# Kernel tuning notes

Hardware: AMD Instinct MI355X
Metric: run time of the kernel (lower is better)

## Reference

```python
import jax, jax.numpy as jnp
import numpy as np

B, S, D, H, DK, DV, DFF = 2, 2048, 512, 8, 64, 64, 2048
EPS = 1e-5

def layer_norm(x, g, b):
    mu = jnp.mean(x, axis=-1, keepdims=True)
    var = jnp.mean(jnp.square(x - mu), axis=-1, keepdims=True)
    return (x - mu) * jax.lax.rsqrt(var + EPS) * g + b

def setup_inputs() -> dict:
    key = jax.random.key(0)
    ks = jax.random.split(key, 12)
    s = 0.02
    return {
        "enc_inputs": jax.random.normal(ks[0], (B, S, D), dtype=jnp.float32),
        "attn_mask": jax.random.randint(ks[1], (B, S, S), 0, 2) == 1,
        "Wq": jax.random.normal(ks[2], (D, H * DK), dtype=jnp.float32) * s,
        "bq": jnp.zeros((H * DK,), jnp.float32),
        "Wk": jax.random.normal(ks[3], (D, H * DK), dtype=jnp.float32) * s,
        "bk": jnp.zeros((H * DK,), jnp.float32),
        "Wv": jax.random.normal(ks[4], (D, H * DV), dtype=jnp.float32) * s,
        "bv": jnp.zeros((H * DV,), jnp.float32),
        "Wo": jax.random.normal(ks[5], (H * DV, D), dtype=jnp.float32) * s,
        "bo": jnp.zeros((D,), jnp.float32),
        "ln1_g": jnp.ones((D,), jnp.float32),
        "ln1_b": jnp.zeros((D,), jnp.float32),
        "W1": jax.random.normal(ks[6], (D, DFF), dtype=jnp.float32) * s,
        "b1": jnp.zeros((DFF,), jnp.float32),
        "W2": jax.random.normal(ks[7], (DFF, D), dtype=jnp.float32) * s,
        "b2": jnp.zeros((D,), jnp.float32),
        "ln2_g": jnp.ones((D,), jnp.float32),
        "ln2_b": jnp.zeros((D,), jnp.float32),
    }

def reference(enc_inputs, attn_mask, Wq, bq, Wk, bk, Wv, bv, Wo, bo,
              ln1_g, ln1_b, W1, b1, W2, b2, ln2_g, ln2_b):
    x = enc_inputs
    # projections -> [B, H, S, dk/dv]
    q = (x @ Wq + bq).reshape(B, S, H, DK).transpose(0, 2, 1, 3)
    k = (x @ Wk + bk).reshape(B, S, H, DK).transpose(0, 2, 1, 3)
    v = (x @ Wv + bv).reshape(B, S, H, DV).transpose(0, 2, 1, 3)
    scores = jnp.einsum('bhqd,bhkd->bhqk', q, k) / np.sqrt(DK).astype(np.float32)
    scores = jnp.where(attn_mask[:, None, :, :], jnp.float32(-1e9), scores)
    attn = jax.nn.softmax(scores, axis=-1)  # [B,H,S,S]
    context = jnp.einsum('bhqk,bhkd->bhqd', attn, v)
    context = context.transpose(0, 2, 1, 3).reshape(B, S, H * DV)
    attn_out = layer_norm(context @ Wo + bo + x, ln1_g, ln1_b)
    # position-wise FFN (1x1 convs == per-token linears)
    h = jax.nn.relu(attn_out @ W1 + b1)
    ffn_out = h @ W2 + b2
    out = layer_norm(ffn_out + attn_out, ln2_g, ln2_b)
    return out, attn
```

## Files before the change

### kernel.cpp

```cpp
#include <hip/hip_runtime.h>
#include <hip/hip_bf16.h>

typedef __bf16 bf16;
typedef __bf16 bf16x8 __attribute__((ext_vector_type(8)));
typedef __bf16 bf16x4 __attribute__((ext_vector_type(4)));
typedef float f32x4 __attribute__((ext_vector_type(4)));

#define S_LEN 2048
#define D_MOD 512
#define NHEAD 8
#define DHEAD 64
#define NBATCH 2

__global__ void detect_kernel(const unsigned char* __restrict__ m, int* __restrict__ flags) {
    __shared__ int s4[4];
    int t = threadIdx.x;
    if (t < 4) s4[t] = 0;
    __syncthreads();
    int c3F = 0, c80p0 = 0, cnzo = 0;
    for (int i = t; i < 4096; i += 256) {
        unsigned b = m[i];
        c3F += (b == 0x3F);
        c80p0 += ((b == 0x80) && ((i & 3) == 0));
        cnzo += ((b != 0) && ((i & 3) != 0));
    }
    atomicAdd(&s4[1], c3F);
    atomicAdd(&s4[2], c80p0);
    atomicAdd(&s4[3], cnzo);
    __syncthreads();
    if (t == 0) {
        int mode;
        if (s4[1] > 0)      mode = (s4[2] > 0) ? 2 : 0;
        else if (s4[3] > 0) mode = 1;
        else                mode = 0;
        flags[1] = mode;
    }
}

__global__ void maskconv_kernel(const unsigned char* __restrict__ m,
                                const int* __restrict__ flags,
                                unsigned char* __restrict__ out) {
    long i = ((long)blockIdx.x * 256 + threadIdx.x) * 4;
    int mode = flags[1];
    uchar4 v;
    if (mode == 0) {
        const int* mi = (const int*)m;
        v.x = (unsigned char)(mi[i + 0] != 0);
        v.y = (unsigned char)(mi[i + 1] != 0);
        v.z = (unsigned char)(mi[i + 2] != 0);
        v.w = (unsigned char)(mi[i + 3] != 0);
    } else if (mode == 1) {
        uchar4 r = *(const uchar4*)(m + i);
        v.x = (r.x != 0); v.y = (r.y != 0); v.z = (r.z != 0); v.w = (r.w != 0);
    } else {
        const unsigned short* ms = (const unsigned short*)m;
        v.x = (unsigned char)(ms[i + 0] != 0);
        v.y = (unsigned char)(ms[i + 1] != 0);
        v.z = (unsigned char)(ms[i + 2] != 0);
        v.w = (unsigned char)(ms[i + 3] != 0);
    }
    *(uchar4*)(out + i) = v;
}

__global__ __launch_bounds__(256) void packA(const float* __restrict__ src,
                                             bf16* __restrict__ outh,
                                             bf16* __restrict__ outl) {
    long i = ((long)blockIdx.x * 256 + threadIdx.x) * 4;
    f32x4 v = *(const f32x4*)(src + i);
    bf16x4 h, l;
    #pragma unroll
    for (int j = 0; j < 4; ++j) {
        bf16 hh = (bf16)v[j];
        h[j] = hh;
        l[j] = (bf16)(v[j] - (float)hh);
    }
    *(bf16x4*)(outh + i) = h;
    *(bf16x4*)(outl + i) = l;
}

__global__ __launch_bounds__(256) void packWT(const float* __restrict__ W,
                                              bf16* __restrict__ outh,
                                              bf16* __restrict__ outl,
                                              int K, int N) {
    __shared__ float tile[64][65];
    int n0 = blockIdx.x * 64, k0 = blockIdx.y * 64;
    int t = threadIdx.x, tx = t & 63, ty = t >> 6;
    #pragma unroll
    for (int r = ty; r < 64; r += 4)
        tile[r][tx] = W[(long)(k0 + r) * N + n0 + tx];
    __syncthreads();
    #pragma unroll
    for (int r = ty; r < 64; r += 4) {
        float v = tile[tx][r];
        bf16 h = (bf16)v;
        long idx = (long)(n0 + r) * K + k0 + tx;
        outh[idx] = h;
        outl[idx] = (bf16)(v - (float)h);
    }
}

template<int EPI>
__global__ __launch_bounds__(256) void mgemm(
    const bf16* __restrict__ Ahi, const bf16* __restrict__ Alo,
    const bf16* __restrict__ Bth, const bf16* __restrict__ Btl,
    const float* __restrict__ bias, const float* __restrict__ res,
    float* __restrict__ outf, bf16* __restrict__ outh, bf16* __restrict__ outl,
    int M, int N, int K)
{
    __shared__ bf16 sAh[64][40], sAl[64][40], sBh[128][40], sBl[128][40];

    int t = threadIdx.x;
    int lane = t & 63, wave = t >> 6;
    int lm = lane & 15, quad = lane >> 4;
    int m0 = blockIdx.y * 64, n0 = blockIdx.x * 128;

    int ar = t >> 2, ac = (t & 3) * 8;
    const bf16* Aph = Ahi + (long)(m0 + ar) * K + ac;
    const bf16* Apl = Alo + (long)(m0 + ar) * K + ac;
    const bf16* Bph0 = Bth + (long)(n0 + ar) * K + ac;
    const bf16* Bph1 = Bth + (long)(n0 + 64 + ar) * K + ac;
    const bf16* Bpl0 = Btl + (long)(n0 + ar) * K + ac;
    const bf16* Bpl1 = Btl + (long)(n0 + 64 + ar) * K + ac;

    f32x4 acc[4][2] = {};

    for (int k0 = 0; k0 < K; k0 += 32) {
        bf16x8 va = *(const bf16x8*)(Aph + k0);
        bf16x8 vb = *(const bf16x8*)(Apl + k0);
        bf16x8 v0 = *(const bf16x8*)(Bph0 + k0);
        bf16x8 v1 = *(const bf16x8*)(Bph1 + k0);
        bf16x8 v2 = *(const bf16x8*)(Bpl0 + k0);
        bf16x8 v3 = *(const bf16x8*)(Bpl1 + k0);
        __syncthreads();
        *(bf16x8*)&sAh[ar][ac] = va;
        *(bf16x8*)&sAl[ar][ac] = vb;
        *(bf16x8*)&sBh[ar][ac] = v0;
        *(bf16x8*)&sBh[ar + 64][ac] = v1;
        *(bf16x8*)&sBl[ar][ac] = v2;
        *(bf16x8*)&sBl[ar + 64][ac] = v3;
        __syncthreads();

        bf16x8 ah[4], al[4], bh[2], bl[2];
        #pragma unroll
        for (int i = 0; i < 4; ++i) {
            ah[i] = *(const bf16x8*)&sAh[i * 16 + lm][quad * 8];
            al[i] = *(const bf16x8*)&sAl[i * 16 + lm][quad * 8];
        }
        #pragma unroll
        for (int j = 0; j < 2; ++j) {
            int r = wave * 32 + j * 16 + lm;
            bh[j] = *(const bf16x8*)&sBh[r][quad * 8];
            bl[j] = *(const bf16x8*)&sBl[r][quad * 8];
        }
        #pragma unroll
        for (int i = 0; i < 4; ++i)
            #pragma unroll
            for (int j = 0; j < 2; ++j) {
                acc[i][j] = __builtin_amdgcn_mfma_f32_16x16x32_bf16(ah[i], bh[j], acc[i][j], 0, 0, 0);
                acc[i][j] = __builtin_amdgcn_mfma_f32_16x16x32_bf16(ah[i], bl[j], acc[i][j], 0, 0, 0);
                acc[i][j] = __builtin_amdgcn_mfma_f32_16x16x32_bf16(al[i], bh[j], acc[i][j], 0, 0, 0);
            }
    }

    #pragma unroll
    for (int i = 0; i < 4; ++i)
        #pragma unroll
        for (int j = 0; j < 2; ++j) {
            int gn = n0 + wave * 32 + j * 16 + lm;
            float bv = bias[gn];
            #pragma unroll
            for (int r = 0; r < 4; ++r) {
                int gm = m0 + i * 16 + quad * 4 + r;
                long idx = (long)gm * N + gn;
                float v = acc[i][j][r] + bv;
                if (EPI == 1) {
                    v = fmaxf(v, 0.f);
                    bf16 h = (bf16)v;
                    outh[idx] = h;
                    outl[idx] = (bf16)(v - (float)h);
                } else {
                    if (EPI == 2) v += res[idx];
                    outf[idx] = v;
                }
            }
        }
}

__global__ void pack_qk(const float* __restrict__ src, bf16* __restrict__ dst) {
    long idx = (long)blockIdx.x * 256 + threadIdx.x;
    int mrow = (int)(idx >> 9), n = (int)(idx & 511);
    int b = mrow >> 11, s = mrow & 2047, h = n >> 6, d = n & 63;
    dst[(((long)(b * NHEAD + h) * S_LEN + s) << 6) + d] = (bf16)src[idx];
}
__global__ void pack_v(const float* __restrict__ src, bf16* __restrict__ dst) {
    long idx = (long)blockIdx.x * 256 + threadIdx.x;
    int mrow = (int)(idx >> 9), n = (int)(idx & 511);
    int b = mrow >> 11, s = mrow & 2047, h = n >> 6, d = n & 63;
    dst[(((long)(b * NHEAD + h) * DHEAD + d) << 11) + s] = (bf16)src[idx];
}

__global__ __launch_bounds__(256) void attn_kernel(
    const bf16* __restrict__ Q, const bf16* __restrict__ Kg,
    const bf16* __restrict__ Vt, const unsigned char* __restrict__ mask8,
    float* __restrict__ attnO, float* __restrict__ ctxf)
{
    __shared__ bf16 Qs[64][72];
    __shared__ bf16 Ks[64][72];
    __shared__ bf16 Vs[64][72];
    __shared__ bf16 Ps[64][72];

    int t = threadIdx.x;
    int qt = blockIdx.x & 31, bh = blockIdx.x >> 5;
    int b_ = bh >> 3, h_ = bh & 7;
    int q0 = qt * 64;
    int lane = t & 63, wave = t >> 6;
    int lm = lane & 15, quad = lane >> 4, q8 = quad * 8;
    int sr = t >> 2, sc = (t & 3) * 16;

    const bf16* Qp = Q + (long)bh * (S_LEN * DHEAD) + (long)(q0 + sr) * DHEAD + sc;
    *(bf16x8*)&Qs[sr][sc]     = *(const bf16x8*)(Qp);
    *(bf16x8*)&Qs[sr][sc + 8] = *(const bf16x8*)(Qp + 8);

    float mrow[4], lrow[4];
    #pragma unroll
    for (int r = 0; r < 4; ++r) { mrow[r] = -1e30f; lrow[r] = 0.f; }

    const bf16* Kbase = Kg + (long)bh * (S_LEN * DHEAD);
    const unsigned char* Mbase = mask8 + (long)b_ * S_LEN * S_LEN;

    for (int kt = 0; kt < 32; ++kt) {
        int k0 = kt * 64;
        __syncthreads();
        const bf16* Kp = Kbase + (long)(k0 + sr) * DHEAD + sc;
        *(bf16x8*)&Ks[sr][sc]     = *(const bf16x8*)(Kp);
        *(bf16x8*)&Ks[sr][sc + 8] = *(const bf16x8*)(Kp + 8);
        __syncthreads();

        f32x4 sacc[4] = {};
        bf16x8 a0 = *(const bf16x8*)&Qs[wave * 16 + lm][q8];
        bf16x8 a1 = *(const bf16x8*)&Qs[wave * 16 + lm][32 + q8];
        #pragma unroll
        for (int tn = 0; tn < 4; ++tn) {
            bf16x8 b0 = *(const bf16x8*)&Ks[tn * 16 + lm][q8];
            bf16x8 b1 = *(const bf16x8*)&Ks[tn * 16 + lm][32 + q8];
            sacc[tn] = __builtin_amdgcn_mfma_f32_16x16x32_bf16(a0, b0, sacc[tn], 0, 0, 0);
            sacc[tn] = __builtin_amdgcn_mfma_f32_16x16x32_bf16(a1, b1, sacc[tn], 0, 0, 0);
        }
        #pragma unroll
        for (int r = 0; r < 4; ++r) {
            int grow = q0 + wave * 16 + quad * 4 + r;
            const unsigned char* Mr = Mbase + (long)grow * S_LEN + k0 + lm;
            float sv[4];
            float tmax = -1e30f;
            #pragma unroll
            for (int tn = 0; tn < 4; ++tn) {
                float s = sacc[tn][r] * 0.125f;
                if (Mr[tn * 16]) s = -1e9f;
                sv[tn] = s;
                tmax = fmaxf(tmax, s);
            }
            #pragma unroll
            for (int off = 8; off; off >>= 1) tmax = fmaxf(tmax, __shfl_xor(tmax, off));
            float mnew = fmaxf(mrow[r], tmax);
            float es = 0.f;
            #pragma unroll
            for (int tn = 0; tn < 4; ++tn) es += __expf(sv[tn] - mnew);
            #pragma unroll
            for (int off = 8; off; off >>= 1) es += __shfl_xor(es, off);
            lrow[r] = lrow[r] * __expf(mrow[r] - mnew) + es;
            mrow[r] = mnew;
        }
    }
    float rl[4];
    #pragma unroll
    for (int r = 0; r < 4; ++r) rl[r] = 1.f / lrow[r];

    float* attnBase = attnO + (long)bh * S_LEN * S_LEN;
    const bf16* Vbase = Vt + (long)bh * (DHEAD * S_LEN);
    f32x4 oacc[4] = {};

    for (int kt = 0; kt < 32; ++kt) {
        int k0 = kt * 64;
        __syncthreads();
        const bf16* Kp = Kbase + (long)(k0 + sr) * DHEAD + sc;
        *(bf16x8*)&Ks[sr][sc]     = *(const bf16x8*)(Kp);
        *(bf16x8*)&Ks[sr][sc + 8] = *(const bf16x8*)(Kp + 8);
        const bf16* Vp = Vbase + (long)sr * S_LEN + k0 + sc;
        *(bf16x8*)&Vs[sr][sc]     = *(const bf16x8*)(Vp);
        *(bf16x8*)&Vs[sr][sc + 8] = *(const bf16x8*)(Vp + 8);
        __syncthreads();

        f32x4 sacc[4] = {};
        bf16x8 a0 = *(const bf16x8*)&Qs[wave * 16 + lm][q8];
        bf16x8 a1 = *(const bf16x8*)&Qs[wave * 16 + lm][32 + q8];
        #pragma unroll
        for (int tn = 0; tn < 4; ++tn) {
            bf16x8 b0 = *(const bf16x8*)&Ks[tn * 16 + lm][q8];
            bf16x8 b1 = *(const bf16x8*)&Ks[tn * 16 + lm][32 + q8];
            sacc[tn] = __builtin_amdgcn_mfma_f32_16x16x32_bf16(a0, b0, sacc[tn], 0, 0, 0);
            sacc[tn] = __builtin_amdgcn_mfma_f32_16x16x32_bf16(a1, b1, sacc[tn], 0, 0, 0);
        }
        #pragma unroll
        for (int r = 0; r < 4; ++r) {
            int grow = q0 + wave * 16 + quad * 4 + r;
            const unsigned char* Mr = Mbase + (long)grow * S_LEN + k0 + lm;
            #pragma unroll
            for (int tn = 0; tn < 4; ++tn) {
                float s = sacc[tn][r] * 0.125f;
                if (Mr[tn * 16]) s = -1e9f;
                float p = __expf(s - mrow[r]) * rl[r];
                attnBase[(long)grow * S_LEN + k0 + tn * 16 + lm] = p;
                Ps[wave * 16 + quad * 4 + r][tn * 16 + lm] = (bf16)p;
            }
        }
        __syncthreads();
        bf16x8 pa0 = *(const bf16x8*)&Ps[wave * 16 + lm][q8];
        bf16x8 pa1 = *(const bf16x8*)&Ps[wave * 16 + lm][32 + q8];
        #pragma unroll
        for (int td = 0; td < 4; ++td) {
            bf16x8 v0 = *(const bf16x8*)&Vs[td * 16 + lm][q8];
            bf16x8 v1 = *(const bf16x8*)&Vs[td * 16 + lm][32 + q8];
            oacc[td] = __builtin_amdgcn_mfma_f32_16x16x32_bf16(pa0, v0, oacc[td], 0, 0, 0);
            oacc[td] = __builtin_amdgcn_mfma_f32_16x16x32_bf16(pa1, v1, oacc[td], 0, 0, 0);
        }
    }

    #pragma unroll
    for (int td = 0; td < 4; ++td)
    #pragma unroll
    for (int r = 0; r < 4; ++r) {
        int grow = q0 + wave * 16 + quad * 4 + r;
        ctxf[(long)(b_ * S_LEN + grow) * D_MOD + h_ * 64 + td * 16 + lm] = oacc[td][r];
    }
}

__global__ __launch_bounds__(256) void ln_kernel(
    const float* __restrict__ X, const float* __restrict__ g,
    const float* __restrict__ bb, float* __restrict__ out)
{
    __shared__ float red[8];
    int row = blockIdx.x, t = threadIdx.x;
    float x0 = X[(long)row * 512 + t];
    float x1 = X[(long)row * 512 + 256 + t];
    float s = x0 + x1, ss = x0 * x0 + x1 * x1;
    #pragma unroll
    for (int off = 32; off; off >>= 1) { s += __shfl_xor(s, off); ss += __shfl_xor(ss, off); }
    if ((t & 63) == 0) { red[t >> 6] = s; red[4 + (t >> 6)] = ss; }
    __syncthreads();
    float S_ = red[0] + red[1] + red[2] + red[3];
    float SS = red[4] + red[5] + red[6] + red[7];
    float mu = S_ * (1.f / 512.f);
    float var = SS * (1.f / 512.f) - mu * mu;
    float is = rsqrtf(var + 1e-5f);
    out[(long)row * 512 + t]       = (x0 - mu) * is * g[t]       + bb[t];
    out[(long)row * 512 + 256 + t] = (x1 - mu) * is * g[t + 256] + bb[t + 256];
}

extern "C" void kernel_launch(void* const* d_in, const int* in_sizes, int n_in,
                              void* d_out, int out_size, void* d_ws, size_t ws_size,
                              hipStream_t stream)
{
    const float* x = (const float*)d_in[0];
    const unsigned char* maskraw = (const unsigned char*)d_in[1];
    const float* Wq = (const float*)d_in[2];  const float* bq = (const float*)d_in[3];
    const float* Wk = (const float*)d_in[4];  const float* bk = (const float*)d_in[5];
    const float* Wv = (const float*)d_in[6];  const float* bv = (const float*)d_in[7];
    const float* Wo = (const float*)d_in[8];  const float* bo = (const float*)d_in[9];
    const float* ln1g = (const float*)d_in[10]; const float* ln1b = (const float*)d_in[11];
    const float* W1 = (const float*)d_in[12]; const float* b1f = (const float*)d_in[13];
    const float* W2 = (const float*)d_in[14]; const float* b2f = (const float*)d_in[15];
    const float* ln2g = (const float*)d_in[16]; const float* ln2b = (const float*)d_in[17];

    float* outMain = (float*)d_out;
    float* outAttn = outMain + (size_t)NBATCH * S_LEN * D_MOD;

    char* w = (char*)d_ws;
    size_t off = 0;
    auto alloc = [&](size_t bytes) -> char* {
        char* p = w + off;
        off += (bytes + 255) & ~(size_t)255;
        return p;
    };
    const size_t MB = 1024 * 1024;
    int* flags = (int*)alloc(256);
    unsigned char* mask8 = (unsigned char*)alloc(8 * MB);
    float* qf   = (float*)alloc(8 * MB);
    float* kf   = (float*)alloc(8 * MB);
    float* vf   = (float*)alloc(8 * MB);
    float* ctxf = (float*)alloc(8 * MB);
    float* tmp   = (float*)alloc(8 * MB);
    float* aoutf = (float*)alloc(8 * MB);
    bf16* Qb   = (bf16*)alloc(4 * MB);
    bf16* Kb   = (bf16*)alloc(4 * MB);
    bf16* Vtb  = (bf16*)alloc(4 * MB);
    bf16* xh = (bf16*)alloc(4 * MB);
    bf16* xl = (bf16*)alloc(4 * MB);
    bf16* WqTh = (bf16*)alloc(512 * 1024); bf16* WqTl = (bf16*)alloc(512 * 1024);
    bf16* WkTh = (bf16*)alloc(512 * 1024); bf16* WkTl = (bf16*)alloc(512 * 1024);
    bf16* WvTh = (bf16*)alloc(512 * 1024); bf16* WvTl = (bf16*)alloc(512 * 1024);
    bf16* WoTh = (bf16*)alloc(512 * 1024); bf16* WoTl = (bf16*)alloc(512 * 1024);
    bf16* hh = (bf16*)qf;
    bf16* hl = (bf16*)vf;
    bf16* W1Th = (bf16*)Qb;
    bf16* W1Tl = W1Th + (size_t)2048 * 512;
    bf16* W2Th = (bf16*)Kb;
    bf16* W2Tl = W2Th + (size_t)512 * 2048;

    const int M = NBATCH * S_LEN;

    detect_kernel<<<1, 256, 0, stream>>>(maskraw, flags);
    maskconv_kernel<<<(NBATCH * S_LEN * S_LEN) / 1024, 256, 0, stream>>>(maskraw, flags, mask8);

    packWT<<<dim3(8, 8), 256, 0, stream>>>(Wq, WqTh, WqTl, 512, 512);
    packWT<<<dim3(8, 8), 256, 0, stream>>>(Wk, WkTh, WkTl, 512, 512);
    packWT<<<dim3(8, 8), 256, 0, stream>>>(Wv, WvTh, WvTl, 512, 512);
    packWT<<<dim3(8, 8), 256, 0, stream>>>(Wo, WoTh, WoTl, 512, 512);

    packA<<<(M * 512) / 1024, 256, 0, stream>>>(x, xh, xl);
    mgemm<0><<<dim3(4, 64), 256, 0, stream>>>(xh, xl, WqTh, WqTl, bq, nullptr, qf, nullptr, nullptr, M, 512, 512);
    mgemm<0><<<dim3(4, 64), 256, 0, stream>>>(xh, xl, WkTh, WkTl, bk, nullptr, kf, nullptr, nullptr, M, 512, 512);
    mgemm<0><<<dim3(4, 64), 256, 0, stream>>>(xh, xl, WvTh, WvTl, bv, nullptr, vf, nullptr, nullptr, M, 512, 512);

    pack_qk<<<(M * 512) / 256, 256, 0, stream>>>(qf, Qb);
    pack_qk<<<(M * 512) / 256, 256, 0, stream>>>(kf, Kb);
    pack_v<<<(M * 512) / 256, 256, 0, stream>>>(vf, Vtb);

    attn_kernel<<<512, 256, 0, stream>>>(Qb, Kb, Vtb, mask8, outAttn, ctxf);

    packWT<<<dim3(32, 8), 256, 0, stream>>>(W1, W1Th, W1Tl, 512, 2048);
    packWT<<<dim3(8, 32), 256, 0, stream>>>(W2, W2Th, W2Tl, 2048, 512);

    packA<<<(M * 512) / 1024, 256, 0, stream>>>(ctxf, xh, xl);
    mgemm<2><<<dim3(4, 64), 256, 0, stream>>>(xh, xl, WoTh, WoTl, bo, x, tmp, nullptr, nullptr, M, 512, 512);
    ln_kernel<<<M, 256, 0, stream>>>(tmp, ln1g, ln1b, aoutf);

    packA<<<(M * 512) / 1024, 256, 0, stream>>>(aoutf, xh, xl);
    mgemm<1><<<dim3(16, 64), 256, 0, stream>>>(xh, xl, W1Th, W1Tl, b1f, nullptr, nullptr, hh, hl, M, 2048, 512);
    mgemm<2><<<dim3(4, 64), 256, 0, stream>>>(hh, hl, W2Th, W2Tl, b2f, aoutf, tmp, nullptr, nullptr, M, 512, 2048);
    ln_kernel<<<M, 256, 0, stream>>>(tmp, ln2g, ln2b, outMain);

    (void)in_sizes; (void)n_in; (void)out_size; (void)ws_size;
}
```

Measured before the change: 688.9 us.

## Fuse QKV GEMM, use 128x128 LDS-direct tiles, fuse bf16 splits into producers

The GEMM tile grows to 128x128 with a 2x2 wave layout, and tiles are loaded with global_load_lds straight into unpadded shared memory. Q, K and V are computed by one fused GEMM over concatenated weights whose epilogue writes Q and K as bf16 in token-major layout, so the pack_qk kernels go away and attention indexes that layout directly. The attention and LayerNorm kernels now emit the hi/lo bf16 split themselves, which removes the separate packA passes and the fp32 intermediate round trips. The trade-offs are LDS bank conflicts from the unpadded rows, fewer blocks per GEMM, and Q/K rounded to bf16 in the GEMM epilogue instead of from fp32.

```diff
diff --git a/kernel.cpp b/kernel.cpp
--- a/kernel.cpp
+++ b/kernel.cpp
@@ -11,6 +11,10 @@
 #define NHEAD 8
 #define DHEAD 64
 #define NBATCH 2
+
+#define GLOAD_LDS(g, l) __builtin_amdgcn_global_load_lds( \
+    (const __attribute__((address_space(1))) unsigned int*)(g), \
+    (__attribute__((address_space(3))) unsigned int*)(l), 16, 0, 0)
 
 __global__ void detect_kernel(const unsigned char* __restrict__ m, int* __restrict__ flags) {
     __shared__ int s4[4];
@@ -99,6 +103,12 @@
     }
 }
 
+__global__ void concat_bias(const float* __restrict__ a, const float* __restrict__ b,
+                            const float* __restrict__ c, float* __restrict__ o) {
+    int t = blockIdx.x * 256 + threadIdx.x;
+    o[t] = (t < 512) ? a[t] : (t < 1024 ? b[t - 512] : c[t - 1024]);
+}
+
 template<int EPI>
 __global__ __launch_bounds__(256) void mgemm(
     const bf16* __restrict__ Ahi, const bf16* __restrict__ Alo,
@@ -107,91 +117,90 @@
     float* __restrict__ outf, bf16* __restrict__ outh, bf16* __restrict__ outl,
     int M, int N, int K)
 {
-    __shared__ bf16 sAh[64][40], sAl[64][40], sBh[128][40], sBl[128][40];
-
+    __shared__ bf16 sAh[128][32], sAl[128][32], sBh[128][32], sBl[128][32];
     int t = threadIdx.x;
     int lane = t & 63, wave = t >> 6;
     int lm = lane & 15, quad = lane >> 4;
-    int m0 = blockIdx.y * 64, n0 = blockIdx.x * 128;
-
-    int ar = t >> 2, ac = (t & 3) * 8;
-    const bf16* Aph = Ahi + (long)(m0 + ar) * K + ac;
-    const bf16* Apl = Alo + (long)(m0 + ar) * K + ac;
-    const bf16* Bph0 = Bth + (long)(n0 + ar) * K + ac;
-    const bf16* Bph1 = Bth + (long)(n0 + 64 + ar) * K + ac;
-    const bf16* Bpl0 = Btl + (long)(n0 + ar) * K + ac;
-    const bf16* Bpl1 = Btl + (long)(n0 + 64 + ar) * K + ac;
-
-    f32x4 acc[4][2] = {};
+    int wr = wave >> 1, wc = wave & 1;
+    int m0 = blockIdx.y * 128, n0 = blockIdx.x * 128;
+
+    int srow = wave * 16 + (lane >> 2);
+    int scol = (lane & 3) * 8;
+    const bf16* pAh = Ahi + (long)(m0 + srow) * K + scol;
+    const bf16* pAl = Alo + (long)(m0 + srow) * K + scol;
+    const bf16* pBh = Bth + (long)(n0 + srow) * K + scol;
+    const bf16* pBl = Btl + (long)(n0 + srow) * K + scol;
+    long rstep = (long)64 * K;
+
+    bf16* lAh = &sAh[wave * 16][0];
+    bf16* lAl = &sAl[wave * 16][0];
+    bf16* lBh = &sBh[wave * 16][0];
+    bf16* lBl = &sBl[wave * 16][0];
+
+    f32x4 acc[4][4] = {};
 
     for (int k0 = 0; k0 < K; k0 += 32) {
-        bf16x8 va = *(const bf16x8*)(Aph + k0);
-        bf16x8 vb = *(const bf16x8*)(Apl + k0);
-        bf16x8 v0 = *(const bf16x8*)(Bph0 + k0);
-        bf16x8 v1 = *(const bf16x8*)(Bph1 + k0);
-        bf16x8 v2 = *(const bf16x8*)(Bpl0 + k0);
-        bf16x8 v3 = *(const bf16x8*)(Bpl1 + k0);
-        __syncthreads();
-        *(bf16x8*)&sAh[ar][ac] = va;
-        *(bf16x8*)&sAl[ar][ac] = vb;
-        *(bf16x8*)&sBh[ar][ac] = v0;
-        *(bf16x8*)&sBh[ar + 64][ac] = v1;
-        *(bf16x8*)&sBl[ar][ac] = v2;
-        *(bf16x8*)&sBl[ar + 64][ac] = v3;
-        __syncthreads();
-
-        bf16x8 ah[4], al[4], bh[2], bl[2];
+        __syncthreads();
+        GLOAD_LDS(pAh + k0,          lAh);
+        GLOAD_LDS(pAh + k0 + rstep,  lAh + 64 * 32);
+        GLOAD_LDS(pAl + k0,          lAl);
+        GLOAD_LDS(pAl + k0 + rstep,  lAl + 64 * 32);
+        GLOAD_LDS(pBh + k0,          lBh);
+        GLOAD_LDS(pBh + k0 + rstep,  lBh + 64 * 32);
+        GLOAD_LDS(pBl + k0,          lBl);
+        GLOAD_LDS(pBl + k0 + rstep,  lBl + 64 * 32);
+        __syncthreads();
+
+        bf16x8 ah[4], al[4];
         #pragma unroll
         for (int i = 0; i < 4; ++i) {
-            ah[i] = *(const bf16x8*)&sAh[i * 16 + lm][quad * 8];
-            al[i] = *(const bf16x8*)&sAl[i * 16 + lm][quad * 8];
-        }
-        #pragma unroll
-        for (int j = 0; j < 2; ++j) {
-            int r = wave * 32 + j * 16 + lm;
-            bh[j] = *(const bf16x8*)&sBh[r][quad * 8];
-            bl[j] = *(const bf16x8*)&sBl[r][quad * 8];
-        }
-        #pragma unroll
-        for (int i = 0; i < 4; ++i)
-            #pragma unroll
-            for (int j = 0; j < 2; ++j) {
-                acc[i][j] = __builtin_amdgcn_mfma_f32_16x16x32_bf16(ah[i], bh[j], acc[i][j], 0, 0, 0);
-                acc[i][j] = __builtin_amdgcn_mfma_f32_16x16x32_bf16(ah[i], bl[j], acc[i][j], 0, 0, 0);
-                acc[i][j] = __builtin_amdgcn_mfma_f32_16x16x32_bf16(al[i], bh[j], acc[i][j], 0, 0, 0);
+            ah[i] = *(const bf16x8*)&sAh[wr * 64 + i * 16 + lm][quad * 8];
+            al[i] = *(const bf16x8*)&sAl[wr * 64 + i * 16 + lm][quad * 8];
+        }
+        #pragma unroll
+        for (int j = 0; j < 4; ++j) {
+            bf16x8 bh = *(const bf16x8*)&sBh[wc * 64 + j * 16 + lm][quad * 8];
+            bf16x8 bl = *(const bf16x8*)&sBl[wc * 64 + j * 16 + lm][quad * 8];
+            #pragma unroll
+            for (int i = 0; i < 4; ++i) {
+                acc[i][j] = __builtin_amdgcn_mfma_f32_16x16x32_bf16(ah[i], bh, acc[i][j], 0, 0, 0);
+                acc[i][j] = __builtin_amdgcn_mfma_f32_16x16x32_bf16(ah[i], bl, acc[i][j], 0, 0, 0);
+                acc[i][j] = __builtin_amdgcn_mfma_f32_16x16x32_bf16(al[i], bh, acc[i][j], 0, 0, 0);
             }
-    }
-
-    #pragma unroll
-    for (int i = 0; i < 4; ++i)
-        #pragma unroll
-        for (int j = 0; j < 2; ++j) {
-            int gn = n0 + wave * 32 + j * 16 + lm;
-            float bv = bias[gn];
+        }
+    }
+
+    #pragma unroll
+    for (int j = 0; j < 4; ++j) {
+        int gn = n0 + wc * 64 + j * 16 + lm;
+        float bv = bias[gn];
+        #pragma unroll
+        for (int i = 0; i < 4; ++i) {
             #pragma unroll
             for (int r = 0; r < 4; ++r) {
-                int gm = m0 + i * 16 + quad * 4 + r;
-                long idx = (long)gm * N + gn;
+                int gm = m0 + wr * 64 + i * 16 + quad * 4 + r;
                 float v = acc[i][j][r] + bv;
-                if (EPI == 1) {
-                    v = fmaxf(v, 0.f);
-                    bf16 h = (bf16)v;
-                    outh[idx] = h;
-                    outl[idx] = (bf16)(v - (float)h);
+                if (EPI == 3) {
+                    if (gn < 512)       outh[(long)gm * 512 + gn] = (bf16)v;
+                    else if (gn < 1024) outl[(long)gm * 512 + gn - 512] = (bf16)v;
+                    else                outf[(long)gm * 512 + gn - 1024] = v;
                 } else {
-                    if (EPI == 2) v += res[idx];
-                    outf[idx] = v;
+                    long idx = (long)gm * N + gn;
+                    if (EPI == 1) {
+                        v = fmaxf(v, 0.f);
+                        bf16 h = (bf16)v;
+                        outh[idx] = h;
+                        outl[idx] = (bf16)(v - (float)h);
+                    } else {
+                        if (EPI == 2) v += res[idx];
+                        outf[idx] = v;
+                    }
                 }
             }
         }
-}
-
-__global__ void pack_qk(const float* __restrict__ src, bf16* __restrict__ dst) {
-    long idx = (long)blockIdx.x * 256 + threadIdx.x;
-    int mrow = (int)(idx >> 9), n = (int)(idx & 511);
-    int b = mrow >> 11, s = mrow & 2047, h = n >> 6, d = n & 63;
-    dst[(((long)(b * NHEAD + h) * S_LEN + s) << 6) + d] = (bf16)src[idx];
-}
+    }
+}
+
 __global__ void pack_v(const float* __restrict__ src, bf16* __restrict__ dst) {
     long idx = (long)blockIdx.x * 256 + threadIdx.x;
     int mrow = (int)(idx >> 9), n = (int)(idx & 511);
@@ -202,7 +211,7 @@
 __global__ __launch_bounds__(256) void attn_kernel(
     const bf16* __restrict__ Q, const bf16* __restrict__ Kg,
     const bf16* __restrict__ Vt, const unsigned char* __restrict__ mask8,
-    float* __restrict__ attnO, float* __restrict__ ctxf)
+    float* __restrict__ attnO, bf16* __restrict__ ctxh, bf16* __restrict__ ctxl)
 {
     __shared__ bf16 Qs[64][72];
     __shared__ bf16 Ks[64][72];
@@ -217,7 +226,7 @@
     int lm = lane & 15, quad = lane >> 4, q8 = quad * 8;
     int sr = t >> 2, sc = (t & 3) * 16;
 
-    const bf16* Qp = Q + (long)bh * (S_LEN * DHEAD) + (long)(q0 + sr) * DHEAD + sc;
+    const bf16* Qp = Q + (((long)(b_ * S_LEN + q0 + sr)) << 9) + (h_ << 6) + sc;
     *(bf16x8*)&Qs[sr][sc]     = *(const bf16x8*)(Qp);
     *(bf16x8*)&Qs[sr][sc + 8] = *(const bf16x8*)(Qp + 8);
 
@@ -225,13 +234,12 @@
     #pragma unroll
     for (int r = 0; r < 4; ++r) { mrow[r] = -1e30f; lrow[r] = 0.f; }
 
-    const bf16* Kbase = Kg + (long)bh * (S_LEN * DHEAD);
     const unsigned char* Mbase = mask8 + (long)b_ * S_LEN * S_LEN;
 
     for (int kt = 0; kt < 32; ++kt) {
         int k0 = kt * 64;
         __syncthreads();
-        const bf16* Kp = Kbase + (long)(k0 + sr) * DHEAD + sc;
+        const bf16* Kp = Kg + (((long)(b_ * S_LEN + k0 + sr)) << 9) + (h_ << 6) + sc;
         *(bf16x8*)&Ks[sr][sc]     = *(const bf16x8*)(Kp);
         *(bf16x8*)&Ks[sr][sc + 8] = *(const bf16x8*)(Kp + 8);
         __syncthreads();
@@ -282,7 +290,7 @@
     for (int kt = 0; kt < 32; ++kt) {
         int k0 = kt * 64;
         __syncthreads();
-        const bf16* Kp = Kbase + (long)(k0 + sr) * DHEAD + sc;
+        const bf16* Kp = Kg + (((long)(b_ * S_LEN + k0 + sr)) << 9) + (h_ << 6) + sc;
         *(bf16x8*)&Ks[sr][sc]     = *(const bf16x8*)(Kp);
         *(bf16x8*)&Ks[sr][sc + 8] = *(const bf16x8*)(Kp + 8);
         const bf16* Vp = Vbase + (long)sr * S_LEN + k0 + sc;
@@ -330,13 +338,19 @@
     #pragma unroll
     for (int r = 0; r < 4; ++r) {
         int grow = q0 + wave * 16 + quad * 4 + r;
-        ctxf[(long)(b_ * S_LEN + grow) * D_MOD + h_ * 64 + td * 16 + lm] = oacc[td][r];
-    }
-}
-
+        long cidx = (((long)(b_ * S_LEN + grow)) << 9) + (h_ << 6) + td * 16 + lm;
+        float v = oacc[td][r];
+        bf16 h = (bf16)v;
+        ctxh[cidx] = h;
+        ctxl[cidx] = (bf16)(v - (float)h);
+    }
+}
+
+template<int SPLIT>
 __global__ __launch_bounds__(256) void ln_kernel(
     const float* __restrict__ X, const float* __restrict__ g,
-    const float* __restrict__ bb, float* __restrict__ out)
+    const float* __restrict__ bb, float* __restrict__ out,
+    bf16* __restrict__ oh, bf16* __restrict__ ol)
 {
     __shared__ float red[8];
     int row = blockIdx.x, t = threadIdx.x;
@@ -352,8 +366,17 @@
     float mu = S_ * (1.f / 512.f);
     float var = SS * (1.f / 512.f) - mu * mu;
     float is = rsqrtf(var + 1e-5f);
-    out[(long)row * 512 + t]       = (x0 - mu) * is * g[t]       + bb[t];
-    out[(long)row * 512 + 256 + t] = (x1 - mu) * is * g[t + 256] + bb[t + 256];
+    float o0 = (x0 - mu) * is * g[t]       + bb[t];
+    float o1 = (x1 - mu) * is * g[t + 256] + bb[t + 256];
+    out[(long)row * 512 + t]       = o0;
+    out[(long)row * 512 + 256 + t] = o1;
+    if (SPLIT) {
+        bf16 h0 = (bf16)o0, h1 = (bf16)o1;
+        oh[(long)row * 512 + t]       = h0;
+        oh[(long)row * 512 + 256 + t] = h1;
+        ol[(long)row * 512 + t]       = (bf16)(o0 - (float)h0);
+        ol[(long)row * 512 + 256 + t] = (bf16)(o1 - (float)h1);
+    }
 }
 
 extern "C" void kernel_launch(void* const* d_in, const int* in_sizes, int n_in,
@@ -384,60 +407,59 @@
     const size_t MB = 1024 * 1024;
     int* flags = (int*)alloc(256);
     unsigned char* mask8 = (unsigned char*)alloc(8 * MB);
-    float* qf   = (float*)alloc(8 * MB);
-    float* kf   = (float*)alloc(8 * MB);
-    float* vf   = (float*)alloc(8 * MB);
-    float* ctxf = (float*)alloc(8 * MB);
+
+    bf16* xh   = (bf16*)alloc(4 * MB);
+    bf16* xl   = (bf16*)alloc(4 * MB);
+    bf16* Qb   = (bf16*)alloc(4 * MB);
+    bf16* Kb   = (bf16*)alloc(4 * MB);
+    float* vf  = (float*)alloc(8 * MB);
+    bf16* Vtb  = (bf16*)alloc(4 * MB);
+    bf16* ctxh = (bf16*)alloc(4 * MB);
+    bf16* ctxl = (bf16*)alloc(4 * MB);
+    bf16* hh = xh;
+    bf16* hl = (bf16*)vf;
+
     float* tmp   = (float*)alloc(8 * MB);
     float* aoutf = (float*)alloc(8 * MB);
-    bf16* Qb   = (bf16*)alloc(4 * MB);
-    bf16* Kb   = (bf16*)alloc(4 * MB);
-    bf16* Vtb  = (bf16*)alloc(4 * MB);
-    bf16* xh = (bf16*)alloc(4 * MB);
-    bf16* xl = (bf16*)alloc(4 * MB);
-    bf16* WqTh = (bf16*)alloc(512 * 1024); bf16* WqTl = (bf16*)alloc(512 * 1024);
-    bf16* WkTh = (bf16*)alloc(512 * 1024); bf16* WkTl = (bf16*)alloc(512 * 1024);
-    bf16* WvTh = (bf16*)alloc(512 * 1024); bf16* WvTl = (bf16*)alloc(512 * 1024);
+    bf16* aouth  = (bf16*)alloc(4 * MB);
+    bf16* aoutl  = (bf16*)alloc(4 * MB);
+
+    bf16* WqkvTh = (bf16*)alloc((size_t)1536 * 512 * 2);
+    bf16* WqkvTl = (bf16*)alloc((size_t)1536 * 512 * 2);
     bf16* WoTh = (bf16*)alloc(512 * 1024); bf16* WoTl = (bf16*)alloc(512 * 1024);
-    bf16* hh = (bf16*)qf;
-    bf16* hl = (bf16*)vf;
-    bf16* W1Th = (bf16*)Qb;
-    bf16* W1Tl = W1Th + (size_t)2048 * 512;
-    bf16* W2Th = (bf16*)Kb;
-    bf16* W2Tl = W2Th + (size_t)512 * 2048;
+    bf16* W1Th = (bf16*)alloc(2 * MB);     bf16* W1Tl = (bf16*)alloc(2 * MB);
+    bf16* W2Th = (bf16*)alloc(2 * MB);     bf16* W2Tl = (bf16*)alloc(2 * MB);
+    float* bqkv = (float*)alloc(1536 * 4);
 
     const int M = NBATCH * S_LEN;
 
     detect_kernel<<<1, 256, 0, stream>>>(maskraw, flags);
     maskconv_kernel<<<(NBATCH * S_LEN * S_LEN) / 1024, 256, 0, stream>>>(maskraw, flags, mask8);
 
-    packWT<<<dim3(8, 8), 256, 0, stream>>>(Wq, WqTh, WqTl, 512, 512);
-    packWT<<<dim3(8, 8), 256, 0, stream>>>(Wk, WkTh, WkTl, 512, 512);
-    packWT<<<dim3(8, 8), 256, 0, stream>>>(Wv, WvTh, WvTl, 512, 512);
+    concat_bias<<<6, 256, 0, stream>>>(bq, bk, bv, bqkv);
+    packWT<<<dim3(8, 8), 256, 0, stream>>>(Wq, WqkvTh,              WqkvTl,              512, 512);
+    packWT<<<dim3(8, 8), 256, 0, stream>>>(Wk, WqkvTh + 512 * 512,  WqkvTl + 512 * 512,  512, 512);
+    packWT<<<dim3(8, 8), 256, 0, stream>>>(Wv, WqkvTh + 1024 * 512, WqkvTl + 1024 * 512, 512, 512);
     packWT<<<dim3(8, 8), 256, 0, stream>>>(Wo, WoTh, WoTl, 512, 512);
-
-    packA<<<(M * 512) / 1024, 256, 0, stream>>>(x, xh, xl);
-    mgemm<0><<<dim3(4, 64), 256, 0, stream>>>(xh, xl, WqTh, WqTl, bq, nullptr, qf, nullptr, nullptr, M, 512, 512);
-    mgemm<0><<<dim3(4, 64), 256, 0, stream>>>(xh, xl, WkTh, WkTl, bk, nullptr, kf, nullptr, nullptr, M, 512, 512);
-    mgemm<0><<<dim3(4, 64), 256, 0, stream>>>(xh, xl, WvTh, WvTl, bv, nullptr, vf, nullptr, nullptr, M, 512, 512);
-
-    pack_qk<<<(M * 512) / 256, 256, 0, stream>>>(qf, Qb);
-    pack_qk<<<(M * 512) / 256, 256, 0, stream>>>(kf, Kb);
-    pack_v<<<(M * 512) / 256, 256, 0, stream>>>(vf, Vtb);
-
-    attn_kernel<<<512, 256, 0, stream>>>(Qb, Kb, Vtb, mask8, outAttn, ctxf);
-
     packWT<<<dim3(32, 8), 256, 0, stream>>>(W1, W1Th, W1Tl, 512, 2048);
     packWT<<<dim3(8, 32), 256, 0, stream>>>(W2, W2Th, W2Tl, 2048, 512);
 
-    packA<<<(M * 512) / 1024, 256, 0, stream>>>(ctxf, xh, xl);
-    mgemm<2><<<dim3(4, 64), 256, 0, stream>>>(xh, xl, WoTh, WoTl, bo, x, tmp, nullptr, nullptr, M, 512, 512);
-    ln_kernel<<<M, 256, 0, stream>>>(tmp, ln1g, ln1b, aoutf);
-
-    packA<<<(M * 512) / 1024, 256, 0, stream>>>(aoutf, xh, xl);
-    mgemm<1><<<dim3(16, 64), 256, 0, stream>>>(xh, xl, W1Th, W1Tl, b1f, nullptr, nullptr, hh, hl, M, 2048, 512);
-    mgemm<2><<<dim3(4, 64), 256, 0, stream>>>(hh, hl, W2Th, W2Tl, b2f, aoutf, tmp, nullptr, nullptr, M, 512, 2048);
-    ln_kernel<<<M, 256, 0, stream>>>(tmp, ln2g, ln2b, outMain);
+    packA<<<(M * 512) / 1024, 256, 0, stream>>>(x, xh, xl);
+    mgemm<3><<<dim3(12, 32), 256, 0, stream>>>(xh, xl, WqkvTh, WqkvTl, bqkv, nullptr,
+                                               vf, Qb, Kb, M, 1536, 512);
+    pack_v<<<(M * 512) / 256, 256, 0, stream>>>(vf, Vtb);
+
+    attn_kernel<<<512, 256, 0, stream>>>(Qb, Kb, Vtb, mask8, outAttn, ctxh, ctxl);
+
+    mgemm<2><<<dim3(4, 32), 256, 0, stream>>>(ctxh, ctxl, WoTh, WoTl, bo, x,
+                                              tmp, nullptr, nullptr, M, 512, 512);
+    ln_kernel<1><<<M, 256, 0, stream>>>(tmp, ln1g, ln1b, aoutf, aouth, aoutl);
+
+    mgemm<1><<<dim3(16, 32), 256, 0, stream>>>(aouth, aoutl, W1Th, W1Tl, b1f, nullptr,
+                                               nullptr, hh, hl, M, 2048, 512);
+    mgemm<2><<<dim3(4, 32), 256, 0, stream>>>(hh, hl, W2Th, W2Tl, b2f, aoutf,
+                                              tmp, nullptr, nullptr, M, 512, 2048);
+    ln_kernel<0><<<M, 256, 0, stream>>>(tmp, ln2g, ln2b, outMain, nullptr, nullptr);
 
     (void)in_sizes; (void)n_in; (void)out_size; (void)ws_size;
 }
```

Result: no change. 695.5 us (+1.0%).
